# Optimization experiments

Measured on AMD Instinct MI355X. Metric: run time of the kernel, lower is better.

## Reference

```python
import jax, jax.numpy as jnp
import numpy as np

P_DROP = 0.1
KEEP = 1.0 - P_DROP
N_DROPOUT_LAYERS = 10  # module stacks 10 Dropout layers per MC sample


def setup_inputs() -> dict:
    key = jax.random.key(0)
    ks = jax.random.split(key, 5)
    B, D_IN, H1, H2 = 32768, 512, 128, 64
    s1 = 1.0 / np.sqrt(D_IN)
    s2 = 1.0 / np.sqrt(H1)
    return {
        "x": jax.random.normal(ks[0], (B, D_IN), dtype=jnp.float32),
        "W1": jax.random.normal(ks[1], (D_IN, H1), dtype=jnp.float32) * s1,
        "b1": jnp.zeros((H1,), dtype=jnp.float32),
        "Wam": jax.random.normal(ks[2], (H1, H2), dtype=jnp.float32) * s2,
        "bam": jnp.zeros((H2,), dtype=jnp.float32),
        "Wav": jax.random.normal(ks[3], (H1, H2), dtype=jnp.float32) * s2,
        "bav": jnp.zeros((H2,), dtype=jnp.float32),
        "We": jax.random.normal(ks[4], (H1, H2), dtype=jnp.float32) * s2,
        "be": jnp.zeros((H2,), dtype=jnp.float32),
        "mc_samples": 10,
    }


def reference(x, W1, b1, Wam, bam, Wav, bav, We, be, mc_samples):
    # shared: Linear -> ReLU -> Dropout (training-mode dropout, inverted scaling)
    kd = jax.random.key(42)
    k_shared, k_mc = jax.random.split(kd)
    h = jax.nn.relu(x @ W1 + b1)  # [B, H1]
    mask_s = jax.random.bernoulli(k_shared, KEEP, h.shape).astype(h.dtype) / KEEP
    h = h * mask_s

    # aleatoric heads
    a_mean = h @ Wam + bam                      # [B, H2]
    a_var = jnp.exp(h @ Wav + bav)              # [B, H2]

    # epistemic: 10 stacked Dropout(p) layers == one dropout with keep prob KEEP**10
    keep_eff = KEEP ** N_DROPOUT_LAYERS
    mask_mc = jax.random.bernoulli(
        k_mc, keep_eff, (mc_samples,) + h.shape
    ).astype(h.dtype) / keep_eff                # [M, B, H1]
    mc_out = jnp.einsum("mbh,hf->mbf", h[None, :, :] * mask_mc, We) + be  # [M, B, H2]
    e_mean = mc_out.mean(axis=0)
    e_var = mc_out.var(axis=0, ddof=1)          # torch.var is unbiased by default
    return (a_mean, a_var, e_mean, e_var)
```

## Files before the change

### kernel.cpp

```cpp
#include <hip/hip_runtime.h>
#include <math.h>
#include <stdint.h>

#define NB   32768
#define DIN  512
#define NH1  128
#define NH2  64
#define NMC  10

__host__ __device__ __forceinline__ uint32_t rotl32(uint32_t x, uint32_t r) {
  return (x << r) | (x >> (32u - r));
}

__host__ __device__ __forceinline__ void tf2x32(uint32_t k0, uint32_t k1,
                                                uint32_t x0, uint32_t x1,
                                                uint32_t& o0, uint32_t& o1) {
  const uint32_t ks2 = k0 ^ k1 ^ 0x1BD11BDAu;
  x0 += k0; x1 += k1;
#define TF_RND(r) { x0 += x1; x1 = rotl32(x1, r); x1 ^= x0; }
  TF_RND(13u) TF_RND(15u) TF_RND(26u) TF_RND(6u)
  x0 += k1;  x1 += ks2 + 1u;
  TF_RND(17u) TF_RND(29u) TF_RND(16u) TF_RND(24u)
  x0 += ks2; x1 += k0 + 2u;
  TF_RND(13u) TF_RND(15u) TF_RND(26u) TF_RND(6u)
  x0 += k0;  x1 += k1 + 3u;
  TF_RND(17u) TF_RND(29u) TF_RND(16u) TF_RND(24u)
  x0 += k1;  x1 += ks2 + 4u;
  TF_RND(13u) TF_RND(15u) TF_RND(26u) TF_RND(6u)
  x0 += ks2; x1 += k0 + 5u;
#undef TF_RND
  o0 = x0; o1 = x1;
}

__device__ __forceinline__ uint32_t rb_part(uint32_t k0, uint32_t k1, uint32_t idx) {
  uint32_t a, b;
  tf2x32(k0, k1, 0u, idx, a, b);
  return a ^ b;
}

__device__ __forceinline__ float bits_to_uniform(uint32_t bits) {
  return __uint_as_float((bits >> 9) | 0x3f800000u) - 1.0f;
}

__global__ __launch_bounds__(256) void k1_gemm_h(
    const float* __restrict__ x, const float* __restrict__ W1,
    const float* __restrict__ b1, const float* __restrict__ Wam,
    const float* __restrict__ bam, const float* __restrict__ Wav,
    const float* __restrict__ bav,
    float* __restrict__ hout, float* __restrict__ out,
    uint32_t s0, uint32_t s1)
{
  __shared__ float xs[32][68];
  __shared__ float w1s[32][132];
  __shared__ float hs[64][128];

  const int tid = threadIdx.x;
  const int b0  = blockIdx.x * 64;
  const int tr  = tid >> 4;
  const int tc  = tid & 15;

  float acc[4][8];
#pragma unroll
  for (int i = 0; i < 4; ++i)
#pragma unroll
    for (int j = 0; j < 8; ++j) acc[i][j] = 0.0f;

  for (int kt = 0; kt < DIN; kt += 32) {
    {
      const int rr = tid >> 3;
      const int cg = tid & 7;
#pragma unroll
      for (int l = 0; l < 2; ++l) {
        float4 v = *(const float4*)(x + (size_t)(b0 + rr + 32 * l) * DIN + kt + cg * 4);
        xs[cg * 4 + 0][rr + 32 * l] = v.x;
        xs[cg * 4 + 1][rr + 32 * l] = v.y;
        xs[cg * 4 + 2][rr + 32 * l] = v.z;
        xs[cg * 4 + 3][rr + 32 * l] = v.w;
      }
#pragma unroll
      for (int l = 0; l < 4; ++l) {
        int idx = tid + l * 256;
        int r2  = idx >> 5;
        int c4  = (idx & 31) * 4;
        *(float4*)&w1s[r2][c4] = *(const float4*)(W1 + (size_t)(kt + r2) * NH1 + c4);
      }
    }
    __syncthreads();
#pragma unroll 8
    for (int kk = 0; kk < 32; ++kk) {
      float a[4], bb[8];
      *(float4*)a        = *(const float4*)&xs[kk][tr * 4];
      *(float4*)&bb[0]   = *(const float4*)&w1s[kk][tc * 8];
      *(float4*)&bb[4]   = *(const float4*)&w1s[kk][tc * 8 + 4];
#pragma unroll
      for (int i = 0; i < 4; ++i)
#pragma unroll
        for (int j = 0; j < 8; ++j)
          acc[i][j] = fmaf(a[i], bb[j], acc[i][j]);
    }
    __syncthreads();
  }

  const float inv_s = 1.0f / 0.9f;
  float hv[4][8];
#pragma unroll
  for (int i = 0; i < 4; ++i) {
    const int row = b0 + tr * 4 + i;
#pragma unroll
    for (int j = 0; j < 8; ++j) {
      const int col = tc * 8 + j;
      float v = acc[i][j] + b1[col];
      v = fmaxf(v, 0.0f);
      uint32_t bits = rb_part(s0, s1, (uint32_t)(row * NH1 + col));
      float u = bits_to_uniform(bits);
      hv[i][j] = (u < 0.9f) ? v * inv_s : 0.0f;
    }
  }
#pragma unroll
  for (int i = 0; i < 4; ++i) {
    const int row = b0 + tr * 4 + i;
    *(float4*)&hs[tr * 4 + i][tc * 8]     = *(float4*)&hv[i][0];
    *(float4*)&hs[tr * 4 + i][tc * 8 + 4] = *(float4*)&hv[i][4];
    *(float4*)(hout + (size_t)row * NH1 + tc * 8)     = *(float4*)&hv[i][0];
    *(float4*)(hout + (size_t)row * NH1 + tc * 8 + 4) = *(float4*)&hv[i][4];
  }
  __syncthreads();

  const int f = tid & 63;
  const int g = tid >> 6;
  float am[16], av[16];
#pragma unroll
  for (int r = 0; r < 16; ++r) { am[r] = 0.0f; av[r] = 0.0f; }
#pragma unroll 4
  for (int k = 0; k < NH1; ++k) {
    const float wa = Wam[k * NH2 + f];
    const float wv = Wav[k * NH2 + f];
#pragma unroll
    for (int r = 0; r < 16; ++r) {
      const float h = hs[r * 4 + g][k];
      am[r] = fmaf(h, wa, am[r]);
      av[r] = fmaf(h, wv, av[r]);
    }
  }
  const float bamf = bam[f], bavf = bav[f];
#pragma unroll
  for (int r = 0; r < 16; ++r) {
    const int row = b0 + r * 4 + g;
    out[(size_t)row * NH2 + f]                       = am[r] + bamf;
    out[(size_t)NB * NH2 + (size_t)row * NH2 + f]    = expf(av[r] + bavf);
  }
}

__global__ __launch_bounds__(256) void k2_mc(
    const float* __restrict__ hin, const float* __restrict__ We,
    const float* __restrict__ be, float* __restrict__ out,
    uint32_t m0, uint32_t m1, float p_mc, float inv_mc)
{
  __shared__ float wes[NH1][NH2 + 1];
  __shared__ float hs2[4][NH1];
  __shared__ float hms[4][NH1][12];

  const int tid = threadIdx.x;
  const int b0  = blockIdx.x * 4;

  for (int idx = tid; idx < NH1 * NH2; idx += 256)
    wes[idx >> 6][idx & 63] = We[idx];
#pragma unroll
  for (int l = 0; l < 2; ++l) {
    const int idx = tid + l * 256;
    hs2[idx >> 7][idx & 127] = hin[(size_t)(b0 + (idx >> 7)) * NH1 + (idx & 127)];
  }
  __syncthreads();

#pragma unroll
  for (int l = 0; l < 2; ++l) {
    const int e  = tid + l * 256;
    const int r2 = e >> 7;
    const int k  = e & 127;
    const uint32_t base = (uint32_t)((b0 + r2) * NH1 + k);
    const float hvmul = hs2[r2][k] * inv_mc;
#pragma unroll
    for (int mm = 0; mm < NMC; ++mm) {
      uint32_t bits = rb_part(m0, m1, base + (uint32_t)mm * (uint32_t)(NB * NH1));
      float u = bits_to_uniform(bits);
      hms[r2][k][mm] = (u < p_mc) ? hvmul : 0.0f;
    }
  }
  __syncthreads();

  const int f = tid & 63;
  const int r = tid >> 6;
  float o[NMC];
#pragma unroll
  for (int m = 0; m < NMC; ++m) o[m] = 0.0f;

#pragma unroll 2
  for (int k = 0; k < NH1; ++k) {
    const float w = wes[k][f];
    const float* hp = &hms[r][k][0];
    float4 h0 = *(const float4*)hp;
    float4 h1 = *(const float4*)(hp + 4);
    float2 h2 = *(const float2*)(hp + 8);
    o[0] = fmaf(h0.x, w, o[0]);  o[1] = fmaf(h0.y, w, o[1]);
    o[2] = fmaf(h0.z, w, o[2]);  o[3] = fmaf(h0.w, w, o[3]);
    o[4] = fmaf(h1.x, w, o[4]);  o[5] = fmaf(h1.y, w, o[5]);
    o[6] = fmaf(h1.z, w, o[6]);  o[7] = fmaf(h1.w, w, o[7]);
    o[8] = fmaf(h2.x, w, o[8]);  o[9] = fmaf(h2.y, w, o[9]);
  }

  const float bef = be[f];
  float s = 0.0f;
#pragma unroll
  for (int m = 0; m < NMC; ++m) { o[m] += bef; s += o[m]; }
  const float mean = s / 10.0f;
  float var = 0.0f;
#pragma unroll
  for (int m = 0; m < NMC; ++m) { const float d = o[m] - mean; var = fmaf(d, d, var); }
  var /= 9.0f;

  const int row = b0 + r;
  out[(size_t)2 * NB * NH2 + (size_t)row * NH2 + f] = mean;
  out[(size_t)3 * NB * NH2 + (size_t)row * NH2 + f] = var;
}

extern "C" void kernel_launch(void* const* d_in, const int* in_sizes, int n_in,
                              void* d_out, int out_size, void* d_ws, size_t ws_size,
                              hipStream_t stream) {
  const float* x   = (const float*)d_in[0];
  const float* W1  = (const float*)d_in[1];
  const float* b1  = (const float*)d_in[2];
  const float* Wam = (const float*)d_in[3];
  const float* bam = (const float*)d_in[4];
  const float* Wav = (const float*)d_in[5];
  const float* bav = (const float*)d_in[6];
  const float* We  = (const float*)d_in[7];
  const float* be  = (const float*)d_in[8];
  float* out = (float*)d_out;
  float* hws = (float*)d_ws;

  uint32_t s0, s1, m0, m1;
  tf2x32(0u, 42u, 0u, 0u, s0, s1);
  tf2x32(0u, 42u, 0u, 1u, m0, m1);

  const float p_mc  = (float)pow(0.9, 10.0);
  const float inv_mc = 1.0f / p_mc;

  k1_gemm_h<<<dim3(NB / 64), dim3(256), 0, stream>>>(
      x, W1, b1, Wam, bam, Wav, bav, hws, out, s0, s1);
  k2_mc<<<dim3(NB / 4), dim3(256), 0, stream>>>(
      hws, We, be, out, m0, m1, p_mc, inv_mc);
}
```

Before: 255.6 us.

## Pack MC dropout masks into bitfields and drop shared We staging

```diff
diff --git a/kernel.cpp b/kernel.cpp
--- a/kernel.cpp
+++ b/kernel.cpp
@@ -151,40 +151,33 @@
   }
 }
 
-__global__ __launch_bounds__(256) void k2_mc(
+__global__ __launch_bounds__(256, 6) void k2_mc(
     const float* __restrict__ hin, const float* __restrict__ We,
     const float* __restrict__ be, float* __restrict__ out,
-    uint32_t m0, uint32_t m1, float p_mc, float inv_mc)
+    uint32_t m0, uint32_t m1, uint32_t thr_mc, float inv_mc)
 {
-  __shared__ float wes[NH1][NH2 + 1];
-  __shared__ float hs2[4][NH1];
-  __shared__ float hms[4][NH1][12];
+  __shared__ float    hpre[4][NH1];
+  __shared__ uint32_t hbits[4][NH1];
 
   const int tid = threadIdx.x;
   const int b0  = blockIdx.x * 4;
-
-  for (int idx = tid; idx < NH1 * NH2; idx += 256)
-    wes[idx >> 6][idx & 63] = We[idx];
-#pragma unroll
-  for (int l = 0; l < 2; ++l) {
-    const int idx = tid + l * 256;
-    hs2[idx >> 7][idx & 127] = hin[(size_t)(b0 + (idx >> 7)) * NH1 + (idx & 127)];
-  }
-  __syncthreads();
 
 #pragma unroll
   for (int l = 0; l < 2; ++l) {
     const int e  = tid + l * 256;
     const int r2 = e >> 7;
     const int k  = e & 127;
+    const float hv = hin[(size_t)b0 * NH1 + e];
+    hpre[r2][k] = hv * inv_mc;
     const uint32_t base = (uint32_t)((b0 + r2) * NH1 + k);
-    const float hvmul = hs2[r2][k] * inv_mc;
+    uint32_t bits = 0u;
 #pragma unroll
     for (int mm = 0; mm < NMC; ++mm) {
-      uint32_t bits = rb_part(m0, m1, base + (uint32_t)mm * (uint32_t)(NB * NH1));
-      float u = bits_to_uniform(bits);
-      hms[r2][k][mm] = (u < p_mc) ? hvmul : 0.0f;
-    }
+      uint32_t a, b;
+      tf2x32(m0, m1, 0u, base + (uint32_t)mm * 4194304u, a, b);
+      bits |= (((a ^ b) < thr_mc) ? 1u : 0u) << mm;
+    }
+    hbits[r2][k] = bits;
   }
   __syncthreads();
 
@@ -194,18 +187,16 @@
 #pragma unroll
   for (int m = 0; m < NMC; ++m) o[m] = 0.0f;
 
-#pragma unroll 2
+#pragma unroll 4
   for (int k = 0; k < NH1; ++k) {
-    const float w = wes[k][f];
-    const float* hp = &hms[r][k][0];
-    float4 h0 = *(const float4*)hp;
-    float4 h1 = *(const float4*)(hp + 4);
-    float2 h2 = *(const float2*)(hp + 8);
-    o[0] = fmaf(h0.x, w, o[0]);  o[1] = fmaf(h0.y, w, o[1]);
-    o[2] = fmaf(h0.z, w, o[2]);  o[3] = fmaf(h0.w, w, o[3]);
-    o[4] = fmaf(h1.x, w, o[4]);  o[5] = fmaf(h1.y, w, o[5]);
-    o[6] = fmaf(h1.z, w, o[6]);  o[7] = fmaf(h1.w, w, o[7]);
-    o[8] = fmaf(h2.x, w, o[8]);  o[9] = fmaf(h2.y, w, o[9]);
+    const float w = We[k * NH2 + f];
+    const float q = hpre[r][k] * w;
+    const uint32_t bits = __builtin_amdgcn_readfirstlane(hbits[r][k]);
+#pragma unroll
+    for (int m = 0; m < NMC; ++m) {
+      const float sm = ((bits >> m) & 1u) ? 1.0f : 0.0f;
+      o[m] = fmaf(sm, q, o[m]);
+    }
   }
 
   const float bef = be[f];
@@ -242,11 +233,13 @@
   tf2x32(0u, 42u, 0u, 0u, s0, s1);
   tf2x32(0u, 42u, 0u, 1u, m0, m1);
 
-  const float p_mc  = (float)pow(0.9, 10.0);
+  const float p_mc   = (float)pow(0.9, 10.0);
   const float inv_mc = 1.0f / p_mc;
+
+  const uint32_t thr_mc = ((uint32_t)ceil((double)p_mc * 8388608.0)) << 9;
 
   k1_gemm_h<<<dim3(NB / 64), dim3(256), 0, stream>>>(
       x, W1, b1, Wam, bam, Wav, bav, hws, out, s0, s1);
   k2_mc<<<dim3(NB / 4), dim3(256), 0, stream>>>(
-      hws, We, be, out, m0, m1, p_mc, inv_mc);
-}
+      hws, We, be, out, m0, m1, thr_mc, inv_mc);
+}
```

New measurement: 301.3 us. 17.9% more time.
